# Kernel optimization log

Hardware: AMD Instinct MI355X
Metric: run time of the kernel (lower is better)

Reference implementation:

```python
import jax, jax.numpy as jnp
import numpy as np

NUM_HEADS = 12

def setup_inputs() -> dict:
    key = jax.random.key(0)
    k1, k2, k3, k4 = jax.random.split(key, 4)
    B, T, N, C = 8, 16, 196, 768
    x = jax.random.normal(k1, (B, T, N, C), dtype=jnp.float32)
    # qkv Linear (no bias): stored as [C, 3C] so y = x @ W_qkv
    W_qkv = jax.random.normal(k2, (C, 3 * C), dtype=jnp.float32) * (C ** -0.5)
    W_proj = jax.random.normal(k3, (C, C), dtype=jnp.float32) * (C ** -0.5)
    b_proj = jax.random.normal(k4, (C,), dtype=jnp.float32) * 0.02
    return {"x": x, "W_qkv": W_qkv, "W_proj": W_proj, "b_proj": b_proj}

def reference(x, W_qkv, W_proj, b_proj):
    B, T, N, C = x.shape
    H = NUM_HEADS
    hd = C // H
    scale = hd ** -0.5
    # shared QKV projection -> [3, B, T, H, N, hd]
    qkv = (x @ W_qkv).reshape(B, T, N, 3, H, hd).transpose(3, 0, 1, 4, 2, 5)
    q, k, v = qkv[0], qkv[1], qkv[2]
    # spatial attention over N (per frame)
    attn = jax.nn.softmax(jnp.einsum('bthnd,bthmd->bthnm', q, k) * scale, axis=-1)
    x1 = jnp.einsum('bthnm,bthmd->bthnd', attn, v)
    x1 = x1.transpose(0, 1, 3, 2, 4).reshape(B, T, N, C)  # [B,T,N,H,hd]->[B,T,N,C]
    # temporal attention over T (per spatial token): permute to [B,H,N,T,hd]
    q2 = q.transpose(0, 2, 3, 1, 4)
    k2 = k.transpose(0, 2, 3, 1, 4)
    v2 = v.transpose(0, 2, 3, 1, 4)
    attn2 = jax.nn.softmax(jnp.einsum('bhntd,bhnsd->bhnts', q2, k2) * scale, axis=-1)
    x2 = jnp.einsum('bhnts,bhnsd->bhntd', attn2, v2)
    x2 = x2.transpose(0, 3, 2, 1, 4).reshape(B, T, N, C)  # [B,T,N,H,hd]->[B,T,N,C]
    # average the two branches, then output projection
    return ((x1 + x2) * 0.5) @ W_proj + b_proj
```

## Files before the change

kernel.cpp:

```cpp
#include <hip/hip_runtime.h>
#include <cstdint>
#include <cstddef>

typedef unsigned short ushort_t;
typedef unsigned int   uint_t;

#define B_   8
#define T_   16
#define N_   196
#define C_   768
#define H_   12
#define C3_  2304
#define M_   25088

#define NP_  208
#define KS_  72
#define VS_  232
#define PS_  232

#define TS_  40

typedef __attribute__((ext_vector_type(8))) short short8;
typedef __attribute__((ext_vector_type(4))) float floatx4;

__device__ __forceinline__ float bf2f(ushort_t u) {
  return __uint_as_float(((uint_t)u) << 16);
}
__device__ __forceinline__ ushort_t f2bf(float f) {
  uint_t u = __float_as_uint(f);
  u += 0x7FFFu + ((u >> 16) & 1u);
  return (ushort_t)(u >> 16);
}
__device__ __forceinline__ uint_t pack2(float a, float b) {
  return (uint_t)f2bf(a) | ((uint_t)f2bf(b) << 16);
}

__device__ __forceinline__ void gload_lds16(const ushort_t* g, ushort_t* l) {
  __builtin_amdgcn_global_load_lds(
      (const __attribute__((address_space(1))) uint_t*)g,
      (__attribute__((address_space(3))) uint_t*)l, 16, 0, 0);
}

__device__ __forceinline__ void bar() {
  asm volatile("" ::: "memory");
  __builtin_amdgcn_s_barrier();
  __builtin_amdgcn_sched_barrier(0);
}

__global__ void fsta_prep(const float* __restrict__ x,
                          ushort_t* __restrict__ xbf,
                          const float* __restrict__ Wqkv,
                          ushort_t* __restrict__ WtQkv,
                          const float* __restrict__ Wproj,
                          ushort_t* __restrict__ WtProj)
{
  const int bid = blockIdx.x;
  const int tid = threadIdx.x;
  if (bid < 9408) {
    int i = (bid * 256 + tid) * 8;
    const float* f = x + i;
    uint4 u;
    u.x = pack2(f[0], f[1]); u.y = pack2(f[2], f[3]);
    u.z = pack2(f[4], f[5]); u.w = pack2(f[6], f[7]);
    *(uint4*)(xbf + i) = u;
  } else if (bid < 16320) {
    int o = (bid - 9408) * 256 + tid;
    int c = o / 768;
    int r = o - c * 768;
    WtQkv[o] = f2bf(Wqkv[(size_t)r * 2304 + c]);
  } else {
    int o = (bid - 16320) * 256 + tid;
    int c = o / 768;
    int r = o - c * 768;
    WtProj[o] = f2bf(Wproj[(size_t)r * 768 + c]);
  }
}

#define STG(X, rb, bu, xo, kss, t)                                            \
  { _Pragma("unroll") for (int c_ = 0; c_ < 2; ++c_) {                        \
      const ushort_t* g_ = (X) +                                              \
          (size_t)((rb) + c_ * 128 + wv * 16 + srow) * K +                    \
          (t) * 64 + (kss) * 32 + chnk * 8;                                   \
      gload_lds16(g_, &lds[(bu) * 32768 + (xo) + (kss) * 8192 +               \
                           c_ * 4096 + wv * 512]); } }

#define PH(bu, mh, kss, DOB, GUARD, ...)                                      \
  { short8 af[4];                                                             \
    _Pragma("unroll") for (int m2 = 0; m2 < 4; ++m2) {                        \
      int rr = wm * 128 + ((mh) * 4 + m2) * 16 + lrow;                        \
      af[m2] = *(const short8*)&lds[(bu) * 32768 + (kss) * 8192 +             \
                                    rr * 32 + rch8]; }                        \
    if (DOB) {                                                                \
      _Pragma("unroll") for (int n2 = 0; n2 < 4; ++n2) {                      \
        int rr = wn * 64 + n2 * 16 + lrow;                                    \
        bf[n2] = *(const short8*)&lds[(bu) * 32768 + 16384 + (kss) * 8192 +   \
                                      rr * 32 + rch8]; } }                    \
    __VA_ARGS__                                                               \
    GUARD                                                                     \
    bar();                                                                    \
    __builtin_amdgcn_s_setprio(1);                                            \
    _Pragma("unroll") for (int m2 = 0; m2 < 4; ++m2)                          \
      _Pragma("unroll") for (int n2 = 0; n2 < 4; ++n2)                        \
        acc[(mh) * 4 + m2][n2] = __builtin_amdgcn_mfma_f32_16x16x32_bf16(     \
            af[m2], bf[n2], acc[(mh) * 4 + m2][n2], 0, 0, 0);                 \
    __builtin_amdgcn_s_setprio(0);                                            \
    bar(); }

#define GUARD_NONE
#define GUARD4 asm volatile("s_waitcnt vmcnt(4)" ::: "memory");
#define GUARD0 asm volatile("s_waitcnt vmcnt(0)" ::: "memory");

template <typename OutT>
__global__ __launch_bounds__(512) void fsta_gemm256(
    const ushort_t* __restrict__ A1,
    const ushort_t* __restrict__ Bt,
    const float* __restrict__ bias,
    OutT* __restrict__ Cout,
    int Ncols, int K)
{
  __shared__ ushort_t lds[65536];
  const int tid  = threadIdx.x;
  const int lane = tid & 63;
  const int wv   = tid >> 6;
  const int wm   = wv >> 2;
  const int wn   = wv & 3;
  const int lrow = lane & 15;
  const int quad = lane >> 4;
  const int rch8 = (quad ^ (lrow & 3)) * 8;
  const int srow = lane >> 2;
  const int chnk = (lane & 3) ^ (srow & 3);

  const int ntx = gridDim.x;
  const int nwg = ntx * gridDim.y;
  int lin = blockIdx.y * ntx + blockIdx.x;
  {
    int q = nwg >> 3, r = nwg & 7;
    int xcd = lin & 7, off = lin >> 3;
    lin = (xcd < r ? xcd * (q + 1) : r * (q + 1) + (xcd - r) * q) + off;
  }
  const int m0 = (lin % ntx) * 256;
  const int n0 = (lin / ntx) * 256;

  const int NT = K >> 6;
  const int NI = NT >> 1;

  floatx4 acc[8][4];
#pragma unroll
  for (int i = 0; i < 8; ++i)
#pragma unroll
    for (int j = 0; j < 4; ++j)
      acc[i][j] = (floatx4){0.f, 0.f, 0.f, 0.f};

  STG(A1, m0, 0, 0,     0, 0)
  STG(Bt, n0, 0, 16384, 0, 0)
  STG(A1, m0, 0, 0,     1, 0)
  STG(Bt, n0, 0, 16384, 1, 0)
  STG(A1, m0, 1, 0,     0, 1)
  STG(Bt, n0, 1, 16384, 0, 1)
  GUARD4
  bar();

  short8 bf[4];
  for (int i = 0; i < NI; ++i) {
    const int t0 = 2 * i;
    const bool lastI = (i == NI - 1);
    PH(0, 0, 0, 1, GUARD_NONE,
       { STG(A1, m0, 1, 0, 1, t0 + 1) STG(Bt, n0, 1, 16384, 1, t0 + 1) })
    PH(0, 1, 0, 0, GUARD_NONE, )
    PH(0, 0, 1, 1, GUARD_NONE,
       { if (!lastI) { STG(A1, m0, 0, 0, 0, t0 + 2) } })
    PH(0, 1, 1, 0, if (lastI) { GUARD0 } else { GUARD4 },
       { if (!lastI) { STG(Bt, n0, 0, 16384, 0, t0 + 2) } })
    PH(1, 0, 0, 1, GUARD_NONE,
       { if (!lastI) { STG(A1, m0, 0, 0, 1, t0 + 2)
                       STG(Bt, n0, 0, 16384, 1, t0 + 2) } })
    PH(1, 1, 0, 0, GUARD_NONE, )
    PH(1, 0, 1, 1, GUARD_NONE,
       { if (!lastI) { STG(A1, m0, 1, 0, 0, t0 + 3) } })
    PH(1, 1, 1, 0, if (!lastI) { GUARD4 },
       { if (!lastI) { STG(Bt, n0, 1, 16384, 0, t0 + 3) } })
  }

#pragma unroll
  for (int m2 = 0; m2 < 8; ++m2) {
    int row = m0 + wm * 128 + m2 * 16 + quad * 4;
#pragma unroll
    for (int n2 = 0; n2 < 4; ++n2) {
      int col = n0 + wn * 64 + n2 * 16 + lrow;
      float badd = bias ? bias[col] : 0.f;
#pragma unroll
      for (int rr = 0; rr < 4; ++rr) {
        float v = acc[m2][n2][rr] + badd;
        if constexpr (sizeof(OutT) == 4)
          Cout[(size_t)(row + rr) * Ncols + col] = v;
        else
          Cout[(size_t)(row + rr) * Ncols + col] = (OutT)f2bf(v);
      }
    }
  }
}

__global__ __launch_bounds__(512) void fsta_spatial(
    const ushort_t* __restrict__ qkv, ushort_t* __restrict__ x1)
{
  __shared__ ushort_t Ks[NP_ * KS_];
  __shared__ ushort_t Vt[64 * VS_];
  __shared__ ushort_t Ps[8][16 * PS_];
  const int tid = threadIdx.x;
  const int bid = blockIdx.x;
  const int h   = bid % H_;
  const int bt  = bid / H_;
  const size_t rowbase = (size_t)bt * N_ * C3_;
  const int hofs = h * 64;

  for (int idx = tid; idx < N_ * 8; idx += 512) {
    int n = idx >> 3, c = (idx & 7) * 8;
    size_t so = rowbase + (size_t)n * C3_ + hofs + c;
    *(uint4*)&Ks[n * KS_ + c] = *(const uint4*)(qkv + so + 768);
    uint4 v = *(const uint4*)(qkv + so + 1536);
    ushort_t tmp[8];
    *(uint4*)tmp = v;
#pragma unroll
    for (int i = 0; i < 8; ++i) Vt[(c + i) * VS_ + n] = tmp[i];
  }
  for (int idx = tid; idx < 64 * (VS_ - N_); idx += 512) {
    int d = idx / (VS_ - N_), k = N_ + idx % (VS_ - N_);
    Vt[d * VS_ + k] = 0;
  }
  __syncthreads();

  const int lane = tid & 63;
  const int wv   = tid >> 6;
  const int lrow = lane & 15;
  const int quad = lane >> 4;
  const int k8   = quad * 8;

  for (int qt = wv; qt < 13; qt += 8) {
    int qrow = qt * 16 + lrow; if (qrow > N_ - 1) qrow = N_ - 1;
    const ushort_t* qp = qkv + rowbase + (size_t)qrow * C3_ + hofs;
    short8 qf0 = *(const short8*)(qp + k8);
    short8 qf1 = *(const short8*)(qp + 32 + k8);

    floatx4 s[13];
#pragma unroll
    for (int kt = 0; kt < 13; ++kt) {
      const ushort_t* kp = &Ks[(kt * 16 + lrow) * KS_];
      short8 kf0 = *(const short8*)(kp + k8);
      short8 kf1 = *(const short8*)(kp + 32 + k8);
      floatx4 a = (floatx4){0.f, 0.f, 0.f, 0.f};
      a = __builtin_amdgcn_mfma_f32_16x16x32_bf16(qf0, kf0, a, 0, 0, 0);
      a = __builtin_amdgcn_mfma_f32_16x16x32_bf16(qf1, kf1, a, 0, 0, 0);
      s[kt] = a;
    }

    if (lrow >= 4)
      s[12] = (floatx4){-INFINITY, -INFINITY, -INFINITY, -INFINITY};

    float mx[4], sum[4];
#pragma unroll
    for (int r = 0; r < 4; ++r) {
      float m2 = s[0][r];
#pragma unroll
      for (int kt = 1; kt < 13; ++kt) m2 = fmaxf(m2, s[kt][r]);
#pragma unroll
      for (int xm = 1; xm < 16; xm <<= 1) m2 = fmaxf(m2, __shfl_xor(m2, xm, 64));
      mx[r] = m2;
    }
#pragma unroll
    for (int r = 0; r < 4; ++r) {
      float sm = 0.f;
#pragma unroll
      for (int kt = 0; kt < 13; ++kt) {
        float p = __expf((s[kt][r] - mx[r]) * 0.125f);
        s[kt][r] = p;
        sm += p;
      }
#pragma unroll
      for (int xm = 1; xm < 16; xm <<= 1) sm += __shfl_xor(sm, xm, 64);
      sum[r] = sm;
    }

    ushort_t* pw = Ps[wv];
#pragma unroll
    for (int kt = 0; kt < 13; ++kt)
#pragma unroll
      for (int r = 0; r < 4; ++r)
        pw[(quad * 4 + r) * PS_ + kt * 16 + lrow] = f2bf(s[kt][r]);
#pragma unroll
    for (int r = 0; r < 4; ++r)
      pw[(quad * 4 + r) * PS_ + 208 + lrow] = 0;

    floatx4 o[4];
#pragma unroll
    for (int nt = 0; nt < 4; ++nt) o[nt] = (floatx4){0.f, 0.f, 0.f, 0.f};
#pragma unroll
    for (int kt = 0; kt < 7; ++kt) {
      short8 pf = *(const short8*)&pw[lrow * PS_ + kt * 32 + k8];
#pragma unroll
      for (int nt = 0; nt < 4; ++nt) {
        short8 vf = *(const short8*)&Vt[(nt * 16 + lrow) * VS_ + kt * 32 + k8];
        o[nt] = __builtin_amdgcn_mfma_f32_16x16x32_bf16(pf, vf, o[nt], 0, 0, 0);
      }
    }

    float inv[4];
#pragma unroll
    for (int r = 0; r < 4; ++r) inv[r] = 1.f / sum[r];
#pragma unroll
    for (int nt = 0; nt < 4; ++nt) {
#pragma unroll
      for (int r = 0; r < 4; ++r) {
        int qr = qt * 16 + quad * 4 + r;
        if (qr < N_)
          x1[(size_t)(bt * N_ + qr) * C_ + hofs + nt * 16 + lrow] =
              f2bf(o[nt][r] * inv[r]);
      }
    }
  }
}

__global__ __launch_bounds__(256) void fsta_temporal(
    const ushort_t* __restrict__ qkv, ushort_t* __restrict__ xavg)
{
  __shared__ ushort_t Pt[4][16 * TS_];
  __shared__ ushort_t Vw[4][64 * TS_];
  const int tid  = threadIdx.x;
  const int lane = tid & 63;
  const int wv   = tid >> 6;
  const int gw   = blockIdx.x * 4 + wv;
  const int n    = gw % N_;
  const int bh   = gw / N_;
  const int h    = bh % H_;
  const int b    = bh / H_;
  const int hofs = h * 64;
  const int lrow = lane & 15;
  const int quad = lane >> 4;
  const int k8   = quad * 8;

  ushort_t* pw = Pt[wv];
  ushort_t* vw = Vw[wv];

  for (int i = lane; i < 16 * 16; i += 64)
    pw[(i >> 4) * TS_ + 16 + (i & 15)] = 0;
  for (int i = lane; i < 64 * 16; i += 64)
    vw[(i >> 4) * TS_ + 16 + (i & 15)] = 0;

  for (int i = lane; i < 128; i += 64) {
    int s = i >> 3, c8 = (i & 7) * 8;
    size_t vo = ((size_t)((b * T_ + s) * N_ + n)) * C3_ + hofs + 1536 + c8;
    ushort_t tmp[8];
    *(uint4*)tmp = *(const uint4*)(qkv + vo);
#pragma unroll
    for (int j = 0; j < 8; ++j) vw[(c8 + j) * TS_ + s] = tmp[j];
  }

  const size_t ro = ((size_t)((b * T_ + lrow) * N_ + n)) * C3_ + hofs;
  short8 qf0 = *(const short8*)(qkv + ro + k8);
  short8 qf1 = *(const short8*)(qkv + ro + 32 + k8);
  short8 kf0 = *(const short8*)(qkv + ro + 768 + k8);
  short8 kf1 = *(const short8*)(qkv + ro + 800 + k8);

  floatx4 s4 = (floatx4){0.f, 0.f, 0.f, 0.f};
  s4 = __builtin_amdgcn_mfma_f32_16x16x32_bf16(qf0, kf0, s4, 0, 0, 0);
  s4 = __builtin_amdgcn_mfma_f32_16x16x32_bf16(qf1, kf1, s4, 0, 0, 0);

  float inv[4];
#pragma unroll
  for (int r = 0; r < 4; ++r) {
    float m2 = s4[r];
#pragma unroll
    for (int xm = 1; xm < 16; xm <<= 1) m2 = fmaxf(m2, __shfl_xor(m2, xm, 64));
    float p = __expf((s4[r] - m2) * 0.125f);
    float sm = p;
#pragma unroll
    for (int xm = 1; xm < 16; xm <<= 1) sm += __shfl_xor(sm, xm, 64);
    pw[(quad * 4 + r) * TS_ + lrow] = f2bf(p);
    inv[r] = 1.f / sm;
  }

  short8 pf = *(const short8*)&pw[lrow * TS_ + k8];
  floatx4 o[4];
#pragma unroll
  for (int nt = 0; nt < 4; ++nt) {
    short8 vf = *(const short8*)&vw[(nt * 16 + lrow) * TS_ + k8];
    o[nt] = __builtin_amdgcn_mfma_f32_16x16x32_bf16(
        pf, vf, (floatx4){0.f, 0.f, 0.f, 0.f}, 0, 0, 0);
  }

#pragma unroll
  for (int nt = 0; nt < 4; ++nt)
#pragma unroll
    for (int r = 0; r < 4; ++r) {
      int t = quad * 4 + r;
      size_t xo = ((size_t)((b * T_ + t) * N_ + n)) * C_ + hofs + nt * 16 + lrow;
      float prev = bf2f(xavg[xo]);
      xavg[xo] = f2bf(0.5f * (prev + o[nt][r] * inv[r]));
    }
}

extern "C" void kernel_launch(void* const* d_in, const int* in_sizes, int n_in,
                              void* d_out, int out_size, void* d_ws, size_t ws_size,
                              hipStream_t stream)
{
  (void)in_sizes; (void)n_in; (void)out_size; (void)ws_size;
  const float* x     = (const float*)d_in[0];
  const float* Wqkv  = (const float*)d_in[1];
  const float* Wproj = (const float*)d_in[2];
  const float* bproj = (const float*)d_in[3];
  float*    out = (float*)d_out;
  ushort_t* ws  = (ushort_t*)d_ws;

  ushort_t* WtQkv  = ws;
  ushort_t* WtProj = ws + 1769472;
  ushort_t* xbf    = ws + 2359296;
  ushort_t* xavg   = xbf;
  ushort_t* qkv    = ws + 21626880;

  fsta_prep<<<dim3(18624), dim3(256), 0, stream>>>(
      x, xbf, Wqkv, WtQkv, Wproj, WtProj);
  fsta_gemm256<ushort_t><<<dim3(98, 9), dim3(512), 0, stream>>>(
      xbf, WtQkv, (const float*)nullptr, qkv, 2304, 768);
  fsta_spatial<<<dim3(B_ * T_ * H_), dim3(512), 0, stream>>>(qkv, xavg);
  fsta_temporal<<<dim3((B_ * H_ * N_) / 4), dim3(256), 0, stream>>>(qkv, xavg);
  fsta_gemm256<float><<<dim3(98, 3), dim3(512), 0, stream>>>(
      xavg, WtProj, bproj, out, 768, 768);
}
```

Measured before the change: 426.9 us.

## Tile weight transposes, change GEMM LDS swizzle, stage attention outputs via LDS

The weight transpose in the prep kernel now goes through a 32x33 shared-memory tile, so both the global reads and writes are coalesced instead of strided. The GEMM LDS swizzle XOR now uses row bits 1-2 instead of 0-1, intended to reduce bank conflicts on fragment reads. The spatial and temporal attention kernels write their outputs into per-wave LDS buffers first and then store full contiguous 64-element rows, replacing scattered 2-byte global writes. This costs extra LDS space and stores, which can lower occupancy in the spatial kernel; the swizzle change must stay consistent between the staging and read sides.

```diff
diff --git a/kernel.cpp b/kernel.cpp
--- a/kernel.cpp
+++ b/kernel.cpp
@@ -54,6 +54,7 @@
                           const float* __restrict__ Wproj,
                           ushort_t* __restrict__ WtProj)
 {
+  __shared__ float tile[32][33];
   const int bid = blockIdx.x;
   const int tid = threadIdx.x;
   if (bid < 9408) {
@@ -63,17 +64,26 @@
     u.x = pack2(f[0], f[1]); u.y = pack2(f[2], f[3]);
     u.z = pack2(f[4], f[5]); u.w = pack2(f[6], f[7]);
     *(uint4*)(xbf + i) = u;
-  } else if (bid < 16320) {
-    int o = (bid - 9408) * 256 + tid;
-    int c = o / 768;
-    int r = o - c * 768;
-    WtQkv[o] = f2bf(Wqkv[(size_t)r * 2304 + c]);
+    return;
+  }
+  const float* src; ushort_t* dst; int Cc, rt, ct;
+  if (bid < 11136) {
+    int b2 = bid - 9408;
+    src = Wqkv; dst = WtQkv; Cc = 2304; ct = b2 % 72; rt = b2 / 72;
   } else {
-    int o = (bid - 16320) * 256 + tid;
-    int c = o / 768;
-    int r = o - c * 768;
-    WtProj[o] = f2bf(Wproj[(size_t)r * 768 + c]);
-  }
+    int b2 = bid - 11136;
+    src = Wproj; dst = WtProj; Cc = 768; ct = b2 % 24; rt = b2 / 24;
+  }
+  const int tx = tid & 31, ty = tid >> 5;
+#pragma unroll
+  for (int i = 0; i < 4; ++i)
+    tile[ty + i * 8][tx] =
+        src[(size_t)(rt * 32 + ty + i * 8) * Cc + ct * 32 + tx];
+  __syncthreads();
+#pragma unroll
+  for (int i = 0; i < 4; ++i)
+    dst[(size_t)(ct * 32 + ty + i * 8) * 768 + rt * 32 + tx] =
+        f2bf(tile[tx][ty + i * 8]);
 }
 
 #define STG(X, rb, bu, xo, kss, t)                                            \
@@ -126,9 +136,9 @@
   const int wn   = wv & 3;
   const int lrow = lane & 15;
   const int quad = lane >> 4;
-  const int rch8 = (quad ^ (lrow & 3)) * 8;
+  const int rch8 = (quad ^ ((lrow >> 1) & 3)) * 8;
   const int srow = lane >> 2;
-  const int chnk = (lane & 3) ^ (srow & 3);
+  const int chnk = (lane & 3) ^ ((srow >> 1) & 3);
 
   const int ntx = gridDim.x;
   const int nwg = ntx * gridDim.y;
@@ -206,6 +216,7 @@
   __shared__ ushort_t Ks[NP_ * KS_];
   __shared__ ushort_t Vt[64 * VS_];
   __shared__ ushort_t Ps[8][16 * PS_];
+  __shared__ ushort_t Os[8][16 * 64];
   const int tid = threadIdx.x;
   const int bid = blockIdx.x;
   const int h   = bid % H_;
@@ -306,15 +317,17 @@
     float inv[4];
 #pragma unroll
     for (int r = 0; r < 4; ++r) inv[r] = 1.f / sum[r];
-#pragma unroll
-    for (int nt = 0; nt < 4; ++nt) {
-#pragma unroll
-      for (int r = 0; r < 4; ++r) {
-        int qr = qt * 16 + quad * 4 + r;
-        if (qr < N_)
-          x1[(size_t)(bt * N_ + qr) * C_ + hofs + nt * 16 + lrow] =
-              f2bf(o[nt][r] * inv[r]);
-      }
+    ushort_t* ow = Os[wv];
+#pragma unroll
+    for (int nt = 0; nt < 4; ++nt)
+#pragma unroll
+      for (int r = 0; r < 4; ++r)
+        ow[(quad * 4 + r) * 64 + nt * 16 + lrow] = f2bf(o[nt][r] * inv[r]);
+#pragma unroll
+    for (int tr = 0; tr < 16; ++tr) {
+      int qr = qt * 16 + tr;
+      if (qr < N_)
+        x1[(size_t)(bt * N_ + qr) * C_ + hofs + lane] = ow[tr * 64 + lane];
     }
   }
 }
@@ -324,6 +337,7 @@
 {
   __shared__ ushort_t Pt[4][16 * TS_];
   __shared__ ushort_t Vw[4][64 * TS_];
+  __shared__ ushort_t Ot[4][16 * 64];
   const int tid  = threadIdx.x;
   const int lane = tid & 63;
   const int wv   = tid >> 6;
@@ -387,15 +401,20 @@
         pf, vf, (floatx4){0.f, 0.f, 0.f, 0.f}, 0, 0, 0);
   }
 
+  ushort_t* ow = Ot[wv];
 #pragma unroll
   for (int nt = 0; nt < 4; ++nt)
 #pragma unroll
-    for (int r = 0; r < 4; ++r) {
-      int t = quad * 4 + r;
-      size_t xo = ((size_t)((b * T_ + t) * N_ + n)) * C_ + hofs + nt * 16 + lrow;
-      float prev = bf2f(xavg[xo]);
-      xavg[xo] = f2bf(0.5f * (prev + o[nt][r] * inv[r]));
-    }
+    for (int r = 0; r < 4; ++r)
+      ow[(quad * 4 + r) * 64 + nt * 16 + lrow] = f2bf(o[nt][r] * inv[r]);
+
+  const size_t obase = ((size_t)(b * T_) * N_ + n) * C_ + hofs + lane;
+#pragma unroll
+  for (int t = 0; t < T_; ++t) {
+    size_t xo = obase + (size_t)t * (N_ * C_);
+    float prev = bf2f(xavg[xo]);
+    xavg[xo] = f2bf(0.5f * (prev + bf2f(ow[t * 64 + lane])));
+  }
 }
 
 extern "C" void kernel_launch(void* const* d_in, const int* in_sizes, int n_in,
@@ -416,7 +435,7 @@
   ushort_t* xavg   = xbf;
   ushort_t* qkv    = ws + 21626880;
 
-  fsta_prep<<<dim3(18624), dim3(256), 0, stream>>>(
+  fsta_prep<<<dim3(11712), dim3(256), 0, stream>>>(
       x, xbf, Wqkv, WtQkv, Wproj, WtProj);
   fsta_gemm256<ushort_t><<<dim3(98, 9), dim3(512), 0, stream>>>(
       xbf, WtQkv, (const float*)nullptr, qkv, 2304, 768);
```

After: 416.5 us. -2.4%, faster.
